# Kernel optimization log

Hardware: AMD Instinct MI355X
Metric: run time of the kernel (lower is better)

## Reference

```python
import jax, jax.numpy as jnp
import numpy as np

B, L = 131072, 24  # batch size, number of links (= n_dofs, all revolute)


def _skew(v):
    # v: [L, 3] -> [L, 3, 3] cross-product matrices
    zeros = jnp.zeros_like(v[:, 0])
    return jnp.stack([
        jnp.stack([zeros, -v[:, 2], v[:, 1]], axis=-1),
        jnp.stack([v[:, 2], zeros, -v[:, 0]], axis=-1),
        jnp.stack([-v[:, 1], v[:, 0], zeros], axis=-1),
    ], axis=-2)


def setup_inputs() -> dict:
    key = jax.random.key(0)
    k1, k2, k3, k4 = jax.random.split(key, 4)
    q = jax.random.normal(k1, (B, L), dtype=jnp.float32)
    qd = jax.random.normal(k2, (B, L), dtype=jnp.float32)
    axes = jax.random.normal(k3, (L, 3), dtype=jnp.float32)   # joint axes (normalized in reference)
    t_fix = jax.random.normal(k4, (L, 3), dtype=jnp.float32)  # fixed parent->joint translations
    return {"q": q, "qd": qd, "axes": axes, "t_fix": t_fix}


def reference(q, qd, axes, t_fix):
    # Stateless forward kinematics for all links of a serial revolute chain.
    # joint_pose_i = Trans(t_fix_i) @ Rot(axis_i, q_i);  pose_i = pose_{i-1} @ joint_pose_i
    dtype = q.dtype
    a = axes / jnp.linalg.norm(axes, axis=-1, keepdims=True)  # [L,3]
    K = _skew(a)                                              # [L,3,3]
    KK = jnp.einsum('lij,ljk->lik', K, K)
    s = jnp.sin(q)[..., None, None]                           # [B,L,1,1]
    c = jnp.cos(q)[..., None, None]
    I3 = jnp.eye(3, dtype=dtype)
    # Rodrigues: per-joint rotation [B,L,3,3]
    R_joint = I3 + s * K[None] + (1.0 - c) * KK[None]

    def step(carry, x):
        Rp, tp = carry          # parent pose: [B,3,3], [B,3]
        Rj, tf = x              # joint rotation [B,3,3], fixed translation [3]
        tc = tp + jnp.einsum('bij,j->bi', Rp, tf)
        Rc = jnp.einsum('bij,bjk->bik', Rp, Rj)
        return (Rc, tc), (Rc, tc)

    R0 = jnp.broadcast_to(I3, (q.shape[0], 3, 3))
    t0 = jnp.zeros((q.shape[0], 3), dtype=dtype)
    Rj_seq = jnp.moveaxis(R_joint, 1, 0)                      # [L,B,3,3]
    _, (Rs, ts) = jax.lax.scan(step, (R0, t0), (Rj_seq, t_fix))
    Rs = jnp.moveaxis(Rs, 0, 1)                               # [B,L,3,3]
    ts = jnp.moveaxis(ts, 0, 1)                               # [B,L,3]
    top = jnp.concatenate([Rs, ts[..., None]], axis=-1)       # [B,L,3,4]
    bottom = jnp.broadcast_to(jnp.array([0., 0., 0., 1.], dtype=dtype),
                              top.shape[:-2] + (1, 4))
    return jnp.concatenate([top, bottom], axis=-2)            # [B,L,4,4]
```

## Files before the change

### kernel.cpp

```cpp
#include <hip/hip_runtime.h>


typedef float v4 __attribute__((ext_vector_type(4)));

constexpr int L = 24;

__global__ __launch_bounds__(256) void fk_kernel(
    const float* __restrict__ q,
    const float* __restrict__ axes,
    const float* __restrict__ tfix,
    float* __restrict__ out,
    int nb)
{
    __shared__ float s_a[L * 3];
    __shared__ float s_t[L * 3];
    if (threadIdx.x < L) {
        const int l = threadIdx.x;
        float ax = axes[l * 3 + 0], ay = axes[l * 3 + 1], az = axes[l * 3 + 2];
        float inv = rsqrtf(ax * ax + ay * ay + az * az);
        s_a[l * 3 + 0] = ax * inv;
        s_a[l * 3 + 1] = ay * inv;
        s_a[l * 3 + 2] = az * inv;
        s_t[l * 3 + 0] = tfix[l * 3 + 0];
        s_t[l * 3 + 1] = tfix[l * 3 + 1];
        s_t[l * 3 + 2] = tfix[l * 3 + 2];
    }
    __syncthreads();

    const int gtid = blockIdx.x * 256 + threadIdx.x;
    const int b = gtid >> 2;
    const int r = gtid & 3;
    if (b >= nb) return;

    float qv[L];
    {
        const v4* q4 = (const v4*)(q + (size_t)b * L);
        #pragma unroll
        for (int i = 0; i < L / 4; ++i) {
            v4 v = q4[i];
            qv[4 * i + 0] = v.x;
            qv[4 * i + 1] = v.y;
            qv[4 * i + 2] = v.z;
            qv[4 * i + 3] = v.w;
        }
    }

    float Ra = (r == 0) ? 1.f : 0.f;
    float Rb = (r == 1) ? 1.f : 0.f;
    float Rc = (r == 2) ? 1.f : 0.f;
    float t  = (r == 3) ? 1.f : 0.f;

    v4* outp = (v4*)(out + (size_t)b * (L * 16) + r * 4);

    #pragma unroll
    for (int l = 0; l < L; ++l) {
        const float ax = s_a[l * 3 + 0], ay = s_a[l * 3 + 1], az = s_a[l * 3 + 2];
        const float fx = s_t[l * 3 + 0], fy = s_t[l * 3 + 1], fz = s_t[l * 3 + 2];

        float s, c;
        __sincosf(qv[l], &s, &c);
        const float omc = 1.0f - c;

        const float xy = omc * ax * ay;
        const float xz = omc * ax * az;
        const float yz = omc * ay * az;
        const float J00 = c + omc * ax * ax;
        const float J11 = c + omc * ay * ay;
        const float J22 = c + omc * az * az;
        const float J01 = xy - s * az, J10 = xy + s * az;
        const float J02 = xz + s * ay, J20 = xz - s * ay;
        const float J12 = yz - s * ax, J21 = yz + s * ax;

        t += Ra * fx + Rb * fy + Rc * fz;

        const float na = Ra * J00 + Rb * J10 + Rc * J20;
        const float nb_ = Ra * J01 + Rb * J11 + Rc * J21;
        const float nc = Ra * J02 + Rb * J12 + Rc * J22;
        Ra = na; Rb = nb_; Rc = nc;

        v4 row = {Ra, Rb, Rc, t};
        __builtin_nontemporal_store(row, outp + 4 * l);
    }
}

extern "C" void kernel_launch(void* const* d_in, const int* in_sizes, int n_in,
                              void* d_out, int out_size, void* d_ws, size_t ws_size,
                              hipStream_t stream) {
    const float* q    = (const float*)d_in[0];
    const float* axes = (const float*)d_in[2];
    const float* tfix = (const float*)d_in[3];
    float* out = (float*)d_out;

    const int nb = in_sizes[0] / L;
    const long long nthreads = (long long)nb * 4;
    const int grid = (int)((nthreads + 255) / 256);
    fk_kernel<<<grid, 256, 0, stream>>>(q, axes, tfix, out, nb);
}
```

Before: 244.2 us.

## Stage output rows in LDS for fully coalesced contiguous global stores

```diff
diff --git a/kernel.cpp b/kernel.cpp
--- a/kernel.cpp
+++ b/kernel.cpp
@@ -4,8 +4,11 @@
 typedef float v4 __attribute__((ext_vector_type(4)));
 
 constexpr int L = 24;
+constexpr int EW = 384;
+constexpr int EWP = 388;
+constexpr int WAVE_WORDS = 16 * EWP;
 
-__global__ __launch_bounds__(256) void fk_kernel(
+__global__ __launch_bounds__(128) void fk_kernel(
     const float* __restrict__ q,
     const float* __restrict__ axes,
     const float* __restrict__ tfix,
@@ -14,6 +17,8 @@
 {
     __shared__ float s_a[L * 3];
     __shared__ float s_t[L * 3];
+    __shared__ float s_buf[2 * WAVE_WORDS];
+
     if (threadIdx.x < L) {
         const int l = threadIdx.x;
         float ax = axes[l * 3 + 0], ay = axes[l * 3 + 1], az = axes[l * 3 + 2];
@@ -27,59 +32,79 @@
     }
     __syncthreads();
 
-    const int gtid = blockIdx.x * 256 + threadIdx.x;
-    const int b = gtid >> 2;
-    const int r = gtid & 3;
-    if (b >= nb) return;
+    const int tid  = threadIdx.x;
+    const int wave = tid >> 6;
+    const int lane = tid & 63;
+    const int e    = lane >> 2;
+    const int r    = lane & 3;
 
-    float qv[L];
-    {
-        const v4* q4 = (const v4*)(q + (size_t)b * L);
+    const int wave_elem0 = blockIdx.x * 32 + wave * 16;
+    const int b = wave_elem0 + e;
+
+    float* wbuf = s_buf + wave * WAVE_WORDS;
+
+    if (b < nb) {
+        float qv[L];
+        {
+            const v4* q4 = (const v4*)(q + (size_t)b * L);
+            #pragma unroll
+            for (int i = 0; i < L / 4; ++i) {
+                v4 v = q4[i];
+                qv[4 * i + 0] = v.x;
+                qv[4 * i + 1] = v.y;
+                qv[4 * i + 2] = v.z;
+                qv[4 * i + 3] = v.w;
+            }
+        }
+
+        float Ra = (r == 0) ? 1.f : 0.f;
+        float Rb = (r == 1) ? 1.f : 0.f;
+        float Rc = (r == 2) ? 1.f : 0.f;
+        float t  = (r == 3) ? 1.f : 0.f;
+
+        v4* lrow = (v4*)(wbuf + e * EWP + r * 4);
+
         #pragma unroll
-        for (int i = 0; i < L / 4; ++i) {
-            v4 v = q4[i];
-            qv[4 * i + 0] = v.x;
-            qv[4 * i + 1] = v.y;
-            qv[4 * i + 2] = v.z;
-            qv[4 * i + 3] = v.w;
+        for (int l = 0; l < L; ++l) {
+            const float ax = s_a[l * 3 + 0], ay = s_a[l * 3 + 1], az = s_a[l * 3 + 2];
+            const float fx = s_t[l * 3 + 0], fy = s_t[l * 3 + 1], fz = s_t[l * 3 + 2];
+
+            float s, c;
+            __sincosf(qv[l], &s, &c);
+            const float omc = 1.0f - c;
+
+            const float xy = omc * ax * ay;
+            const float xz = omc * ax * az;
+            const float yz = omc * ay * az;
+            const float J00 = c + omc * ax * ax;
+            const float J11 = c + omc * ay * ay;
+            const float J22 = c + omc * az * az;
+            const float J01 = xy - s * az, J10 = xy + s * az;
+            const float J02 = xz + s * ay, J20 = xz - s * ay;
+            const float J12 = yz - s * ax, J21 = yz + s * ax;
+
+            t += Ra * fx + Rb * fy + Rc * fz;
+
+            const float na  = Ra * J00 + Rb * J10 + Rc * J20;
+            const float nb_ = Ra * J01 + Rb * J11 + Rc * J21;
+            const float nc  = Ra * J02 + Rb * J12 + Rc * J22;
+            Ra = na; Rb = nb_; Rc = nc;
+
+            lrow[l * 4] = v4{Ra, Rb, Rc, t};
         }
     }
+    __syncthreads();
 
-    float Ra = (r == 0) ? 1.f : 0.f;
-    float Rb = (r == 1) ? 1.f : 0.f;
-    float Rc = (r == 2) ? 1.f : 0.f;
-    float t  = (r == 3) ? 1.f : 0.f;
-
-    v4* outp = (v4*)(out + (size_t)b * (L * 16) + r * 4);
-
-    #pragma unroll
-    for (int l = 0; l < L; ++l) {
-        const float ax = s_a[l * 3 + 0], ay = s_a[l * 3 + 1], az = s_a[l * 3 + 2];
-        const float fx = s_t[l * 3 + 0], fy = s_t[l * 3 + 1], fz = s_t[l * 3 + 2];
-
-        float s, c;
-        __sincosf(qv[l], &s, &c);
-        const float omc = 1.0f - c;
-
-        const float xy = omc * ax * ay;
-        const float xz = omc * ax * az;
-        const float yz = omc * ay * az;
-        const float J00 = c + omc * ax * ax;
-        const float J11 = c + omc * ay * ay;
-        const float J22 = c + omc * az * az;
-        const float J01 = xy - s * az, J10 = xy + s * az;
-        const float J02 = xz + s * ay, J20 = xz - s * ay;
-        const float J12 = yz - s * ax, J21 = yz + s * ax;
-
-        t += Ra * fx + Rb * fy + Rc * fz;
-
-        const float na = Ra * J00 + Rb * J10 + Rc * J20;
-        const float nb_ = Ra * J01 + Rb * J11 + Rc * J21;
-        const float nc = Ra * J02 + Rb * J12 + Rc * J22;
-        Ra = na; Rb = nb_; Rc = nc;
-
-        v4 row = {Ra, Rb, Rc, t};
-        __builtin_nontemporal_store(row, outp + 4 * l);
+    if (wave_elem0 < nb) {
+        float* gbase = out + (size_t)wave_elem0 * EW;
+        #pragma unroll
+        for (int j = 0; j < 24; ++j) {
+            const unsigned w = (unsigned)(j * 256 + lane * 4);
+            const unsigned elem = w / EW;
+            const unsigned rem  = w - elem * EW;
+            v4 v = *(const v4*)(wbuf + elem * EWP + rem);
+            __builtin_nontemporal_store(v, (v4*)(gbase + w));
+        }
     }
 }
 
@@ -93,6 +118,6 @@
 
     const int nb = in_sizes[0] / L;
     const long long nthreads = (long long)nb * 4;
-    const int grid = (int)((nthreads + 255) / 256);
-    fk_kernel<<<grid, 256, 0, stream>>>(q, axes, tfix, out, nb);
+    const int grid = (int)((nthreads + 127) / 128);
+    fk_kernel<<<grid, 128, 0, stream>>>(q, axes, tfix, out, nb);
 }
```

Result: faster. 221.3 us (-9.4%).
